# Kernel optimization log

Hardware: AMD Instinct MI355X
Metric: run time of the kernel (lower is better)

## Reference

```python
import jax, jax.numpy as jnp
import numpy as np

BN_EPS = 1e-5

def _vq(x, embed):
    # x: (..., dim), embed: (dim, K). Nearest-codeword lookup with straight-through.
    dim = x.shape[-1]
    flat = x.reshape(-1, dim)
    dist = (flat * flat).sum(1, keepdims=True) - 2.0 * (flat @ embed) + (embed * embed).sum(0, keepdims=True)
    ids = jnp.argmin(dist, axis=1)
    q = jnp.take(embed.T, ids, axis=0).reshape(x.shape)
    diff = jnp.mean((jax.lax.stop_gradient(q) - x) ** 2)
    q = x + jax.lax.stop_gradient(q - x)
    return q, diff

def _weight_quantize(W, embed, in_mem, out_mem):
    # W: (out_f, in_f). Group W.T into (out_g, in_g, in_mem*out_mem) blocks,
    # VQ each block, scatter back to (out_f, in_f). Matches torch chunk/stack loops.
    out_f, in_f = W.shape
    in_g, out_g = in_f // in_mem, out_f // out_mem
    g = W.T.reshape(in_g, in_mem, out_g, out_mem).transpose(2, 0, 1, 3).reshape(out_g, in_g, in_mem * out_mem)
    q, diff = _vq(g, embed)
    qW = q.reshape(out_g, in_g, in_mem, out_mem).transpose(0, 3, 1, 2).reshape(out_f, in_f)
    return qW, diff

def _bn(x, gamma, beta):
    # training-mode BatchNorm1d: biased batch variance
    mu = x.mean(axis=0)
    var = ((x - mu) ** 2).mean(axis=0)
    return (x - mu) * jax.lax.rsqrt(var + BN_EPS) * gamma + beta


def setup_inputs() -> dict:
    key = jax.random.key(0)
    ks = jax.random.split(key, 8)
    B, D_IN, H, D_OUT, K = 65536, 784, 512, 10, 512
    s = 0.05
    return {
        "x": jax.random.normal(ks[0], (B, D_IN), jnp.float32),
        "W1": jax.random.normal(ks[1], (H, D_IN), jnp.float32) * s,
        "b1": jnp.zeros((H,), jnp.float32),
        "gamma1": jnp.ones((H,), jnp.float32),
        "beta1": jnp.zeros((H,), jnp.float32),
        "E1": jax.random.normal(ks[2], (28, K), jnp.float32) * s,  # dim = in_mem(7)*out_mem(4)
        "W2": jax.random.normal(ks[3], (H, H), jnp.float32) * s,
        "b2": jnp.zeros((H,), jnp.float32),
        "E2": jax.random.normal(ks[4], (16, K), jnp.float32) * s,  # dim = in_mem(16)*out_mem(1)
        "W3": jax.random.normal(ks[5], (D_OUT, H), jnp.float32) * s,
        "b3": jnp.zeros((D_OUT,), jnp.float32),
    }


def reference(x, W1, b1, gamma1, beta1, E1, W2, b2, E2, W3, b3):
    qW1, diff1 = _weight_quantize(W1, E1, 7, 4)
    h = jax.nn.relu(x @ qW1.T + b1)
    qW2, diff2 = _weight_quantize(W2, E2, 16, 1)
    h = jax.nn.relu(_bn(h, gamma1, beta1) @ qW2.T + b2)
    out = h @ W3.T + b3
    return out, diff1 + diff2
```

## Files before the change

### kernel.cpp

```cpp
#include <hip/hip_runtime.h>
#include <stdint.h>

#define BATCH   65536
#define D_IN    784
#define KP      832
#define HDIM    512
#define D_OUT   10
#define NCODE   512
#define HT_LD   520

typedef _Float16 f16;
typedef _Float16 f16x8 __attribute__((ext_vector_type(8)));
typedef float    f32x4 __attribute__((ext_vector_type(4)));

__device__ __forceinline__ void gld_lds16(const void* g, void* l) {
  __builtin_amdgcn_global_load_lds((const __attribute__((address_space(1))) void*)g,
                                   (__attribute__((address_space(3))) void*)l, 16, 0, 0);
}

#define MEMFENCE asm volatile("" ::: "memory")
#define BARRIER() do { MEMFENCE; __builtin_amdgcn_s_barrier(); MEMFENCE; } while (0)

__global__ void k_vq1(const float* __restrict__ W1, const float* __restrict__ E1,
                      f16* __restrict__ qW1, float* __restrict__ diffacc) {
  #pragma clang fp contract(off)
  __shared__ float E1s[28 * NCODE];
  __shared__ float Ts[NCODE];
  for (int i = threadIdx.x; i < 28 * NCODE; i += 256) E1s[i] = E1[i];
  __syncthreads();
  for (int k = threadIdx.x; k < NCODE; k += 256) {
    float e0 = E1s[k];
    float t = e0 * e0;
    for (int j = 1; j < 28; ++j) {
      float e = E1s[j * NCODE + k];
      float ee = e * e;
      t = t + ee;
    }
    Ts[k] = t;
  }
  __syncthreads();
  const int wid = threadIdx.x >> 6, lane = threadIdx.x & 63;
  const int bid = blockIdx.x * 4 + wid;
  const int og = bid / 112, ig = bid % 112;
  float v[28], vv[28];
  #pragma unroll
  for (int j = 0; j < 28; ++j) {
    int om = j & 3, im = j >> 2;
    v[j] = W1[(og * 4 + om) * D_IN + ig * 7 + im];
    vv[j] = v[j] * v[j];
  }
  float r[8];
  #pragma unroll
  for (int j = 0; j < 8; ++j) r[j] = vv[j];
  #pragma unroll
  for (int j = 0; j < 8; ++j) r[j] = r[j] + vv[8 + j];
  #pragma unroll
  for (int j = 0; j < 8; ++j) r[j] = r[j] + vv[16 + j];
  float s = ((r[0] + r[1]) + (r[2] + r[3])) + ((r[4] + r[5]) + (r[6] + r[7]));
  s = s + vv[24]; s = s + vv[25]; s = s + vv[26]; s = s + vv[27];

  float bestd = 1e30f; int bestk = 0x7fffffff;
  for (int t = 0; t < 8; ++t) {
    int k = t * 64 + lane;
    float dot = 0.f;
    #pragma unroll
    for (int j = 0; j < 28; ++j) dot = __builtin_fmaf(v[j], E1s[j * NCODE + k], dot);
    float d = (s - 2.0f * dot) + Ts[k];
    if (d < bestd || (d == bestd && k < bestk)) { bestd = d; bestk = k; }
  }
  for (int off = 32; off; off >>= 1) {
    float d2 = __shfl_down(bestd, off, 64);
    int   k2 = __shfl_down(bestk, off, 64);
    if (d2 < bestd || (d2 == bestd && k2 < bestk)) { bestd = d2; bestk = k2; }
  }
  int kstar = __shfl(bestk, 0, 64);
  float sq = 0.f;
  if (lane < 28) {
    int om = lane & 3, im = lane >> 2;
    float q = E1s[lane * NCODE + kstar];
    qW1[(size_t)(og * 4 + om) * KP + ig * 7 + im] = (f16)q;
    float dd = q - v[lane]; sq = dd * dd;
  }
  for (int off = 32; off; off >>= 1) sq += __shfl_down(sq, off, 64);
  if (lane == 0) atomicAdd(&diffacc[bid & 127], sq);
}

__global__ void k_vq2(const float* __restrict__ W2, const float* __restrict__ E2,
                      f16* __restrict__ qW2, float* __restrict__ diffacc) {
  #pragma clang fp contract(off)
  __shared__ float E2s[16 * NCODE];
  __shared__ float Ts[NCODE];
  for (int i = threadIdx.x; i < 16 * NCODE; i += 256) E2s[i] = E2[i];
  __syncthreads();
  for (int k = threadIdx.x; k < NCODE; k += 256) {
    float e0 = E2s[k];
    float t = e0 * e0;
    for (int j = 1; j < 16; ++j) {
      float e = E2s[j * NCODE + k];
      float ee = e * e;
      t = t + ee;
    }
    Ts[k] = t;
  }
  __syncthreads();
  const int wid = threadIdx.x >> 6, lane = threadIdx.x & 63;
  const int bid = blockIdx.x * 4 + wid;
  const int og = bid >> 5, ig = bid & 31;
  float v[16], vv[16];
  #pragma unroll
  for (int j = 0; j < 16; ++j) {
    v[j] = W2[og * HDIM + ig * 16 + j];
    vv[j] = v[j] * v[j];
  }
  float r[8];
  #pragma unroll
  for (int j = 0; j < 8; ++j) r[j] = vv[j];
  #pragma unroll
  for (int j = 0; j < 8; ++j) r[j] = r[j] + vv[8 + j];
  float s = ((r[0] + r[1]) + (r[2] + r[3])) + ((r[4] + r[5]) + (r[6] + r[7]));

  float bestd = 1e30f; int bestk = 0x7fffffff;
  for (int t = 0; t < 8; ++t) {
    int k = t * 64 + lane;
    float dot = 0.f;
    #pragma unroll
    for (int j = 0; j < 16; ++j) dot = __builtin_fmaf(v[j], E2s[j * NCODE + k], dot);
    float d = (s - 2.0f * dot) + Ts[k];
    if (d < bestd || (d == bestd && k < bestk)) { bestd = d; bestk = k; }
  }
  for (int off = 32; off; off >>= 1) {
    float d2 = __shfl_down(bestd, off, 64);
    int   k2 = __shfl_down(bestk, off, 64);
    if (d2 < bestd || (d2 == bestd && k2 < bestk)) { bestd = d2; bestk = k2; }
  }
  int kstar = __shfl(bestk, 0, 64);
  float sq = 0.f;
  if (lane < 16) {
    float q = E2s[lane * NCODE + kstar];
    qW2[(size_t)og * HDIM + ig * 16 + lane] = (f16)q;
    float dd = q - v[lane]; sq = dd * dd;
  }
  for (int off = 32; off; off >>= 1) sq += __shfl_down(sq, off, 64);
  if (lane == 0) atomicAdd(&diffacc[bid & 127], sq);
}

__global__ void __launch_bounds__(512, 2)
k_gemm1(const float* __restrict__ X, const f16* __restrict__ Bw,
        const float* __restrict__ bias, f16* __restrict__ C,
        float* __restrict__ statacc) {
  __shared__ __align__(16) char lds_all[147456];
  __shared__ float cls[512], cls2[512];
  f16* ht = (f16*)lds_all;
  const int tid = threadIdx.x;
  const int bm = blockIdx.x;
  const int lane = tid & 63, wid = tid >> 6;
  const int waveM = wid & 1, waveN = wid >> 1;
  const int l15 = lane & 15, quad = lane >> 4;

  cls[tid] = 0.f; cls2[tid] = 0.f;

  const int rA = tid >> 2, cA = tid & 3;
  const float* gArow = X + (size_t)(bm * 128 + rA) * D_IN;
  const int wA0 = rA * 64 + ((cA ^ (rA & 7)) * 8);
  const int wA1 = rA * 64 + (((cA + 4) ^ (rA & 7)) * 8);
  const f16* gBp[8]; int lBoff[8];
  #pragma unroll
  for (int i = 0; i < 8; ++i) {
    int s = tid + i * 512;
    int rB = s >> 3, cB = s & 7;
    gBp[i] = Bw + (size_t)rB * KP + ((cB ^ (rB & 7)) * 8);
    lBoff[i] = s * 8;
  }

  f32x4 acc[4][8];
  #pragma unroll
  for (int i = 0; i < 4; ++i)
    #pragma unroll
    for (int j = 0; j < 8; ++j) acc[i][j] = (f32x4){0.f, 0.f, 0.f, 0.f};

  const int swz = (l15 & 7);
  const int arow = waveM * 64 + l15;
  const int brow = waveN * 128 + l15;

  float4 ra0, ra1, ra2, ra3;
  auto issueA = [&](int k0) {
    int g0 = k0 + cA * 8;
    int g1 = k0 + (cA + 4) * 8;
    int g0c = g0 < D_IN ? g0 : 0;
    int g1c = g1 < D_IN ? g1 : 0;
    ra0 = *(const float4*)(gArow + g0c);
    ra1 = *(const float4*)(gArow + g0c + 4);
    ra2 = *(const float4*)(gArow + g1c);
    ra3 = *(const float4*)(gArow + g1c + 4);
  };
  auto writeA = [&](int k0) {
    float4 a0 = ra0, a1 = ra1, b0 = ra2, b1 = ra3;
    if (k0 + cA * 8 >= D_IN)       { a0 = (float4){0.f,0.f,0.f,0.f}; a1 = a0; }
    if (k0 + (cA + 4) * 8 >= D_IN) { b0 = (float4){0.f,0.f,0.f,0.f}; b1 = b0; }
    f16x8 o0, o1;
    o0[0]=(f16)a0.x; o0[1]=(f16)a0.y; o0[2]=(f16)a0.z; o0[3]=(f16)a0.w;
    o0[4]=(f16)a1.x; o0[5]=(f16)a1.y; o0[6]=(f16)a1.z; o0[7]=(f16)a1.w;
    o1[0]=(f16)b0.x; o1[1]=(f16)b0.y; o1[2]=(f16)b0.z; o1[3]=(f16)b0.w;
    o1[4]=(f16)b1.x; o1[5]=(f16)b1.y; o1[6]=(f16)b1.z; o1[7]=(f16)b1.w;
    *(f16x8*)((f16*)lds_all + wA0) = o0;
    *(f16x8*)((f16*)lds_all + wA1) = o1;
  };
  auto issueB = [&](int k0, int bOff) {
    f16* Bs_ = (f16*)(lds_all + bOff);
    #pragma unroll
    for (int i = 0; i < 8; ++i) gld_lds16(gBp[i] + k0, Bs_ + lBoff[i]);
  };
  auto mma = [&](int bOff) {
    const f16* As_ = (const f16*)lds_all;
    const f16* Bs_ = (const f16*)(lds_all + bOff);
    #pragma unroll
    for (int ks = 0; ks < 2; ++ks) {
      const int coff = ((ks * 4 + quad) ^ swz) * 8;
      f16x8 af[4], bf[8];
      #pragma unroll
      for (int i = 0; i < 4; ++i) af[i] = *(const f16x8*)(As_ + (arow + i * 16) * 64 + coff);
      #pragma unroll
      for (int j = 0; j < 8; ++j) bf[j] = *(const f16x8*)(Bs_ + (brow + j * 16) * 64 + coff);
      #pragma unroll
      for (int i = 0; i < 4; ++i)
        #pragma unroll
        for (int j = 0; j < 8; ++j)
          acc[i][j] = __builtin_amdgcn_mfma_f32_16x16x32_f16(af[i], bf[j], acc[i][j], 0, 0, 0);
    }
  };

  const int NT = KP / 64;
  issueA(0);  MEMFENCE;
  issueB(0, 16384); MEMFENCE;

  for (int k = 0; k < NT; ++k) {
    BARRIER();
    writeA(k * 64);
    MEMFENCE;
    if (k + 1 < NT) {
      issueA((k + 1) * 64); MEMFENCE;
      issueB((k + 1) * 64, 16384 + ((k + 1) & 1) * 65536); MEMFENCE;
      asm volatile("s_waitcnt vmcnt(12) lgkmcnt(0)" ::: "memory");
    } else {
      asm volatile("s_waitcnt vmcnt(0) lgkmcnt(0)" ::: "memory");
    }
    BARRIER();
    __builtin_amdgcn_s_setprio(1);
    mma(16384 + (k & 1) * 65536);
    __builtin_amdgcn_s_setprio(0);
  }
  __syncthreads();

  const int colbase = waveN * 128 + l15;
  float bcol[8];
  #pragma unroll
  for (int j = 0; j < 8; ++j) bcol[j] = bias[colbase + j * 16];
  float cs[8], cs2[8];
  #pragma unroll
  for (int j = 0; j < 8; ++j) { cs[j] = 0.f; cs2[j] = 0.f; }
  #pragma unroll
  for (int i = 0; i < 4; ++i)
    #pragma unroll
    for (int r2 = 0; r2 < 4; ++r2) {
      int rloc = waveM * 64 + i * 16 + quad * 4 + r2;
      #pragma unroll
      for (int j = 0; j < 8; ++j) {
        float v = acc[i][j][r2] + bcol[j];
        v = v > 0.f ? v : 0.f;
        ht[rloc * HT_LD + waveN * 128 + j * 16 + l15] = (f16)v;
        cs[j] += v; cs2[j] += v * v;
      }
    }
  #pragma unroll
  for (int j = 0; j < 8; ++j) {
    cs[j]  += __shfl_xor(cs[j], 16, 64);  cs[j]  += __shfl_xor(cs[j], 32, 64);
    cs2[j] += __shfl_xor(cs2[j], 16, 64); cs2[j] += __shfl_xor(cs2[j], 32, 64);
  }
  if (quad == 0) {
    #pragma unroll
    for (int j = 0; j < 8; ++j) {
      atomicAdd(&cls[waveN * 128 + j * 16 + l15], cs[j]);
      atomicAdd(&cls2[waveN * 128 + j * 16 + l15], cs2[j]);
    }
  }
  __syncthreads();
  atomicAdd(&statacc[256 + tid], cls[tid]);
  atomicAdd(&statacc[768 + tid], cls2[tid]);
  #pragma unroll
  for (int rr = 0; rr < 16; ++rr) {
    int row = wid * 16 + rr;
    f16x8 vrow = *(const f16x8*)(ht + row * HT_LD + lane * 8);
    *(f16x8*)(C + (size_t)(bm * 128 + row) * HDIM + lane * 8) = vrow;
  }
}

__global__ void k_bnprep(const float* __restrict__ acc, const float* __restrict__ gamma,
                         const float* __restrict__ beta, float* __restrict__ ab,
                         const float* __restrict__ W3, f16* __restrict__ W3h,
                         float* __restrict__ diff_out) {
  const int c = threadIdx.x;
  const float inv = 1.f / 65536.f;
  float mu = acc[256 + c] * inv;
  float msq = acc[768 + c] * inv;
  float var = msq - mu * mu;
  float a = gamma[c] / sqrtf(var + 1e-5f);
  ab[c] = a;
  ab[512 + c] = beta[c] - mu * a;
  #pragma unroll
  for (int o = 0; o < 16; ++o)
    W3h[o * HDIM + c] = (o < D_OUT) ? (f16)W3[o * HDIM + c] : (f16)0.f;
  if (c == 0) {
    float s1 = 0.f, s2 = 0.f;
    for (int i = 0; i < 128; ++i) { s1 += acc[i]; s2 += acc[128 + i]; }
    diff_out[0] = s1 * (1.f / 401408.f) + s2 * (1.f / 262144.f);
  }
}

__global__ void k_bnfold(f16* __restrict__ qW2, const float* __restrict__ ab,
                         const float* __restrict__ b2, float* __restrict__ bias2) {
  __shared__ float red[256];
  const int n = blockIdx.x, t = threadIdx.x;
  float partial = 0.f;
  #pragma unroll
  for (int kk = 0; kk < 2; ++kk) {
    int k = t + kk * 256;
    float w = (float)qW2[n * HDIM + k];
    partial += ab[512 + k] * w;
    qW2[n * HDIM + k] = (f16)(ab[k] * w);
  }
  red[t] = partial; __syncthreads();
  for (int s = 128; s > 0; s >>= 1) { if (t < s) red[t] += red[t + s]; __syncthreads(); }
  if (t == 0) bias2[n] = b2[n] + red[0];
}

__global__ void __launch_bounds__(512, 2)
k_gemm2f(const f16* __restrict__ A, const f16* __restrict__ Bw,
         const float* __restrict__ bias2, const f16* __restrict__ W3h,
         const float* __restrict__ b3, float* __restrict__ out) {
  __shared__ __align__(16) char lds_all[147456];
  f16* ht = (f16*)lds_all;
  const int tid = threadIdx.x;
  const int bm = blockIdx.x;
  const int lane = tid & 63, wid = tid >> 6;
  const int waveM = wid & 1, waveN = wid >> 1;
  const int l15 = lane & 15, quad = lane >> 4;

  const int rA = tid >> 2, cA = tid & 3;
  const f16* gArow = A + (size_t)(bm * 128 + rA) * HDIM;
  const int wA0 = rA * 64 + ((cA ^ (rA & 7)) * 8);
  const int wA1 = rA * 64 + (((cA + 4) ^ (rA & 7)) * 8);
  const f16* gBp[8]; int lBoff[8];
  #pragma unroll
  for (int i = 0; i < 8; ++i) {
    int s = tid + i * 512;
    int rB = s >> 3, cB = s & 7;
    gBp[i] = Bw + (size_t)rB * HDIM + ((cB ^ (rB & 7)) * 8);
    lBoff[i] = s * 8;
  }

  f32x4 acc[4][8];
  #pragma unroll
  for (int i = 0; i < 4; ++i)
    #pragma unroll
    for (int j = 0; j < 8; ++j) acc[i][j] = (f32x4){0.f, 0.f, 0.f, 0.f};

  const int swz = (l15 & 7);
  const int arow = waveM * 64 + l15;
  const int brow = waveN * 128 + l15;

  f16x8 ra0, ra1;
  auto issueA = [&](int k0) {
    ra0 = *(const f16x8*)(gArow + k0 + cA * 8);
    ra1 = *(const f16x8*)(gArow + k0 + (cA + 4) * 8);
  };
  auto writeA = [&]() {
    *(f16x8*)((f16*)lds_all + wA0) = ra0;
    *(f16x8*)((f16*)lds_all + wA1) = ra1;
  };
  auto issueB = [&](int k0, int bOff) {
    f16* Bs_ = (f16*)(lds_all + bOff);
    #pragma unroll
    for (int i = 0; i < 8; ++i) gld_lds16(gBp[i] + k0, Bs_ + lBoff[i]);
  };
  auto mma = [&](int bOff) {
    const f16* As_ = (const f16*)lds_all;
    const f16* Bs_ = (const f16*)(lds_all + bOff);
    #pragma unroll
    for (int ks = 0; ks < 2; ++ks) {
      const int coff = ((ks * 4 + quad) ^ swz) * 8;
      f16x8 af[4], bf[8];
      #pragma unroll
      for (int i = 0; i < 4; ++i) af[i] = *(const f16x8*)(As_ + (arow + i * 16) * 64 + coff);
      #pragma unroll
      for (int j = 0; j < 8; ++j) bf[j] = *(const f16x8*)(Bs_ + (brow + j * 16) * 64 + coff);
      #pragma unroll
      for (int i = 0; i < 4; ++i)
        #pragma unroll
        for (int j = 0; j < 8; ++j)
          acc[i][j] = __builtin_amdgcn_mfma_f32_16x16x32_f16(af[i], bf[j], acc[i][j], 0, 0, 0);
    }
  };

  const int NT = HDIM / 64;
  issueA(0);  MEMFENCE;
  issueB(0, 16384); MEMFENCE;

  for (int k = 0; k < NT; ++k) {
    BARRIER();
    writeA();
    MEMFENCE;
    if (k + 1 < NT) {
      issueA((k + 1) * 64); MEMFENCE;
      issueB((k + 1) * 64, 16384 + ((k + 1) & 1) * 65536); MEMFENCE;
      asm volatile("s_waitcnt vmcnt(10) lgkmcnt(0)" ::: "memory");
    } else {
      asm volatile("s_waitcnt vmcnt(0) lgkmcnt(0)" ::: "memory");
    }
    BARRIER();
    __builtin_amdgcn_s_setprio(1);
    mma(16384 + (k & 1) * 65536);
    __builtin_amdgcn_s_setprio(0);
  }
  __syncthreads();

  const int colbase = waveN * 128 + l15;
  float bcol[8];
  #pragma unroll
  for (int j = 0; j < 8; ++j) bcol[j] = bias2[colbase + j * 16];
  #pragma unroll
  for (int i = 0; i < 4; ++i)
    #pragma unroll
    for (int r2 = 0; r2 < 4; ++r2) {
      int rloc = waveM * 64 + i * 16 + quad * 4 + r2;
      #pragma unroll
      for (int j = 0; j < 8; ++j) {
        float v = acc[i][j][r2] + bcol[j];
        v = v > 0.f ? v : 0.f;
        ht[rloc * HT_LD + waveN * 128 + j * 16 + l15] = (f16)v;
      }
    }
  __syncthreads();
  f32x4 oacc = (f32x4){0.f, 0.f, 0.f, 0.f};
  #pragma unroll
  for (int ks = 0; ks < 16; ++ks) {
    f16x8 bfr = *(const f16x8*)(W3h + l15 * HDIM + ks * 32 + quad * 8);
    f16x8 afr = *(const f16x8*)(ht + (wid * 16 + l15) * HT_LD + ks * 32 + quad * 8);
    oacc = __builtin_amdgcn_mfma_f32_16x16x32_f16(afr, bfr, oacc, 0, 0, 0);
  }
  if (l15 < D_OUT) {
    float badd = b3[l15];
    #pragma unroll
    for (int r2 = 0; r2 < 4; ++r2) {
      int row = bm * 128 + wid * 16 + quad * 4 + r2;
      out[(size_t)row * D_OUT + l15] = oacc[r2] + badd;
    }
  }
}

extern "C" void kernel_launch(void* const* d_in, const int* in_sizes, int n_in,
                              void* d_out, int out_size, void* d_ws, size_t ws_size,
                              hipStream_t stream) {
  const float* x     = (const float*)d_in[0];
  const float* W1    = (const float*)d_in[1];
  const float* b1    = (const float*)d_in[2];
  const float* gamma = (const float*)d_in[3];
  const float* beta  = (const float*)d_in[4];
  const float* E1    = (const float*)d_in[5];
  const float* W2    = (const float*)d_in[6];
  const float* b2    = (const float*)d_in[7];
  const float* E2    = (const float*)d_in[8];
  const float* W3    = (const float*)d_in[9];
  const float* b3    = (const float*)d_in[10];
  float* out = (float*)d_out;

  char* ws = (char*)d_ws;
  float* accum = (float*)ws;
  f16* qW1h = (f16*)(ws + 8192);
  f16* qW2h = (f16*)(ws + 860160);
  f16* W3h  = (f16*)(ws + 1384448);
  float* ab = (float*)(ws + 1400832);
  float* bias2 = (float*)(ws + 1404928);
  f16* h    = (f16*)(ws + 1409024);

  (void)hipMemsetAsync(ws, 0, 860160, stream);
  k_vq1<<<3584, 256, 0, stream>>>(W1, E1, qW1h, accum);
  k_vq2<<<4096, 256, 0, stream>>>(W2, E2, qW2h, accum + 128);
  k_gemm1<<<512, 512, 0, stream>>>(x, qW1h, b1, h, accum);
  k_bnprep<<<1, 512, 0, stream>>>(accum, gamma, beta, ab, W3, W3h, out + (size_t)BATCH * D_OUT);
  k_bnfold<<<512, 256, 0, stream>>>(qW2h, ab, b2, bias2);
  k_gemm2f<<<512, 512, 0, stream>>>(h, qW2h, bias2, W3h, b3, out);
}
```

Measured before the change: 515.1 us.

## Merge VQ kernels, fold BN prep into bnfold, finer-grained GEMM pipelining

```diff
diff --git a/kernel.cpp b/kernel.cpp
--- a/kernel.cpp
+++ b/kernel.cpp
@@ -20,128 +20,126 @@
 
 #define MEMFENCE asm volatile("" ::: "memory")
 #define BARRIER() do { MEMFENCE; __builtin_amdgcn_s_barrier(); MEMFENCE; } while (0)
-
-__global__ void k_vq1(const float* __restrict__ W1, const float* __restrict__ E1,
-                      f16* __restrict__ qW1, float* __restrict__ diffacc) {
+#define LGKM0 asm volatile("s_waitcnt lgkmcnt(0)" ::: "memory")
+
+__global__ void k_vq(const float* __restrict__ W1, const float* __restrict__ E1,
+                     f16* __restrict__ qW1,
+                     const float* __restrict__ W2, const float* __restrict__ E2,
+                     f16* __restrict__ qW2, float* __restrict__ diffacc) {
   #pragma clang fp contract(off)
-  __shared__ float E1s[28 * NCODE];
+  __shared__ float Es[28 * NCODE];
   __shared__ float Ts[NCODE];
-  for (int i = threadIdx.x; i < 28 * NCODE; i += 256) E1s[i] = E1[i];
-  __syncthreads();
-  for (int k = threadIdx.x; k < NCODE; k += 256) {
-    float e0 = E1s[k];
-    float t = e0 * e0;
-    for (int j = 1; j < 28; ++j) {
-      float e = E1s[j * NCODE + k];
-      float ee = e * e;
-      t = t + ee;
-    }
-    Ts[k] = t;
-  }
-  __syncthreads();
   const int wid = threadIdx.x >> 6, lane = threadIdx.x & 63;
-  const int bid = blockIdx.x * 4 + wid;
-  const int og = bid / 112, ig = bid % 112;
-  float v[28], vv[28];
-  #pragma unroll
-  for (int j = 0; j < 28; ++j) {
-    int om = j & 3, im = j >> 2;
-    v[j] = W1[(og * 4 + om) * D_IN + ig * 7 + im];
-    vv[j] = v[j] * v[j];
-  }
-  float r[8];
-  #pragma unroll
-  for (int j = 0; j < 8; ++j) r[j] = vv[j];
-  #pragma unroll
-  for (int j = 0; j < 8; ++j) r[j] = r[j] + vv[8 + j];
-  #pragma unroll
-  for (int j = 0; j < 8; ++j) r[j] = r[j] + vv[16 + j];
-  float s = ((r[0] + r[1]) + (r[2] + r[3])) + ((r[4] + r[5]) + (r[6] + r[7]));
-  s = s + vv[24]; s = s + vv[25]; s = s + vv[26]; s = s + vv[27];
-
-  float bestd = 1e30f; int bestk = 0x7fffffff;
-  for (int t = 0; t < 8; ++t) {
-    int k = t * 64 + lane;
-    float dot = 0.f;
-    #pragma unroll
-    for (int j = 0; j < 28; ++j) dot = __builtin_fmaf(v[j], E1s[j * NCODE + k], dot);
-    float d = (s - 2.0f * dot) + Ts[k];
-    if (d < bestd || (d == bestd && k < bestk)) { bestd = d; bestk = k; }
-  }
-  for (int off = 32; off; off >>= 1) {
-    float d2 = __shfl_down(bestd, off, 64);
-    int   k2 = __shfl_down(bestk, off, 64);
-    if (d2 < bestd || (d2 == bestd && k2 < bestk)) { bestd = d2; bestk = k2; }
-  }
-  int kstar = __shfl(bestk, 0, 64);
-  float sq = 0.f;
-  if (lane < 28) {
-    int om = lane & 3, im = lane >> 2;
-    float q = E1s[lane * NCODE + kstar];
-    qW1[(size_t)(og * 4 + om) * KP + ig * 7 + im] = (f16)q;
-    float dd = q - v[lane]; sq = dd * dd;
-  }
-  for (int off = 32; off; off >>= 1) sq += __shfl_down(sq, off, 64);
-  if (lane == 0) atomicAdd(&diffacc[bid & 127], sq);
-}
-
-__global__ void k_vq2(const float* __restrict__ W2, const float* __restrict__ E2,
-                      f16* __restrict__ qW2, float* __restrict__ diffacc) {
-  #pragma clang fp contract(off)
-  __shared__ float E2s[16 * NCODE];
-  __shared__ float Ts[NCODE];
-  for (int i = threadIdx.x; i < 16 * NCODE; i += 256) E2s[i] = E2[i];
-  __syncthreads();
-  for (int k = threadIdx.x; k < NCODE; k += 256) {
-    float e0 = E2s[k];
-    float t = e0 * e0;
-    for (int j = 1; j < 16; ++j) {
-      float e = E2s[j * NCODE + k];
-      float ee = e * e;
-      t = t + ee;
-    }
-    Ts[k] = t;
-  }
-  __syncthreads();
-  const int wid = threadIdx.x >> 6, lane = threadIdx.x & 63;
-  const int bid = blockIdx.x * 4 + wid;
-  const int og = bid >> 5, ig = bid & 31;
-  float v[16], vv[16];
-  #pragma unroll
-  for (int j = 0; j < 16; ++j) {
-    v[j] = W2[og * HDIM + ig * 16 + j];
-    vv[j] = v[j] * v[j];
-  }
-  float r[8];
-  #pragma unroll
-  for (int j = 0; j < 8; ++j) r[j] = vv[j];
-  #pragma unroll
-  for (int j = 0; j < 8; ++j) r[j] = r[j] + vv[8 + j];
-  float s = ((r[0] + r[1]) + (r[2] + r[3])) + ((r[4] + r[5]) + (r[6] + r[7]));
-
-  float bestd = 1e30f; int bestk = 0x7fffffff;
-  for (int t = 0; t < 8; ++t) {
-    int k = t * 64 + lane;
-    float dot = 0.f;
-    #pragma unroll
-    for (int j = 0; j < 16; ++j) dot = __builtin_fmaf(v[j], E2s[j * NCODE + k], dot);
-    float d = (s - 2.0f * dot) + Ts[k];
-    if (d < bestd || (d == bestd && k < bestk)) { bestd = d; bestk = k; }
-  }
-  for (int off = 32; off; off >>= 1) {
-    float d2 = __shfl_down(bestd, off, 64);
-    int   k2 = __shfl_down(bestk, off, 64);
-    if (d2 < bestd || (d2 == bestd && k2 < bestk)) { bestd = d2; bestk = k2; }
-  }
-  int kstar = __shfl(bestk, 0, 64);
-  float sq = 0.f;
-  if (lane < 16) {
-    float q = E2s[lane * NCODE + kstar];
-    qW2[(size_t)og * HDIM + ig * 16 + lane] = (f16)q;
-    float dd = q - v[lane]; sq = dd * dd;
-  }
-  for (int off = 32; off; off >>= 1) sq += __shfl_down(sq, off, 64);
-  if (lane == 0) atomicAdd(&diffacc[bid & 127], sq);
+  if (blockIdx.x < 3584) {
+    for (int i = threadIdx.x; i < 28 * NCODE; i += 256) Es[i] = E1[i];
+    __syncthreads();
+    for (int k = threadIdx.x; k < NCODE; k += 256) {
+      float e0 = Es[k];
+      float t = e0 * e0;
+      for (int j = 1; j < 28; ++j) {
+        float e = Es[j * NCODE + k];
+        float ee = e * e;
+        t = t + ee;
+      }
+      Ts[k] = t;
+    }
+    __syncthreads();
+    const int bid = blockIdx.x * 4 + wid;
+    const int og = bid / 112, ig = bid % 112;
+    float v[28], vv[28];
+    #pragma unroll
+    for (int j = 0; j < 28; ++j) {
+      int om = j & 3, im = j >> 2;
+      v[j] = W1[(og * 4 + om) * D_IN + ig * 7 + im];
+      vv[j] = v[j] * v[j];
+    }
+    float r[8];
+    #pragma unroll
+    for (int j = 0; j < 8; ++j) r[j] = vv[j];
+    #pragma unroll
+    for (int j = 0; j < 8; ++j) r[j] = r[j] + vv[8 + j];
+    #pragma unroll
+    for (int j = 0; j < 8; ++j) r[j] = r[j] + vv[16 + j];
+    float s = ((r[0] + r[1]) + (r[2] + r[3])) + ((r[4] + r[5]) + (r[6] + r[7]));
+    s = s + vv[24]; s = s + vv[25]; s = s + vv[26]; s = s + vv[27];
+
+    float bestd = 1e30f; int bestk = 0x7fffffff;
+    for (int t = 0; t < 8; ++t) {
+      int k = t * 64 + lane;
+      float dot = 0.f;
+      #pragma unroll
+      for (int j = 0; j < 28; ++j) dot = __builtin_fmaf(v[j], Es[j * NCODE + k], dot);
+      float d = (s - 2.0f * dot) + Ts[k];
+      if (d < bestd || (d == bestd && k < bestk)) { bestd = d; bestk = k; }
+    }
+    for (int off = 32; off; off >>= 1) {
+      float d2 = __shfl_down(bestd, off, 64);
+      int   k2 = __shfl_down(bestk, off, 64);
+      if (d2 < bestd || (d2 == bestd && k2 < bestk)) { bestd = d2; bestk = k2; }
+    }
+    int kstar = __shfl(bestk, 0, 64);
+    float sq = 0.f;
+    if (lane < 28) {
+      int om = lane & 3, im = lane >> 2;
+      float q = Es[lane * NCODE + kstar];
+      qW1[(size_t)(og * 4 + om) * KP + ig * 7 + im] = (f16)q;
+      float dd = q - v[lane]; sq = dd * dd;
+    }
+    for (int off = 32; off; off >>= 1) sq += __shfl_down(sq, off, 64);
+    if (lane == 0) atomicAdd(&diffacc[bid & 127], sq);
+  } else {
+    for (int i = threadIdx.x; i < 16 * NCODE; i += 256) Es[i] = E2[i];
+    __syncthreads();
+    for (int k = threadIdx.x; k < NCODE; k += 256) {
+      float e0 = Es[k];
+      float t = e0 * e0;
+      for (int j = 1; j < 16; ++j) {
+        float e = Es[j * NCODE + k];
+        float ee = e * e;
+        t = t + ee;
+      }
+      Ts[k] = t;
+    }
+    __syncthreads();
+    const int bid = (blockIdx.x - 3584) * 4 + wid;
+    const int og = bid >> 5, ig = bid & 31;
+    float v[16], vv[16];
+    #pragma unroll
+    for (int j = 0; j < 16; ++j) {
+      v[j] = W2[og * HDIM + ig * 16 + j];
+      vv[j] = v[j] * v[j];
+    }
+    float r[8];
+    #pragma unroll
+    for (int j = 0; j < 8; ++j) r[j] = vv[j];
+    #pragma unroll
+    for (int j = 0; j < 8; ++j) r[j] = r[j] + vv[8 + j];
+    float s = ((r[0] + r[1]) + (r[2] + r[3])) + ((r[4] + r[5]) + (r[6] + r[7]));
+
+    float bestd = 1e30f; int bestk = 0x7fffffff;
+    for (int t = 0; t < 8; ++t) {
+      int k = t * 64 + lane;
+      float dot = 0.f;
+      #pragma unroll
+      for (int j = 0; j < 16; ++j) dot = __builtin_fmaf(v[j], Es[j * NCODE + k], dot);
+      float d = (s - 2.0f * dot) + Ts[k];
+      if (d < bestd || (d == bestd && k < bestk)) { bestd = d; bestk = k; }
+    }
+    for (int off = 32; off; off >>= 1) {
+      float d2 = __shfl_down(bestd, off, 64);
+      int   k2 = __shfl_down(bestk, off, 64);
+      if (d2 < bestd || (d2 == bestd && k2 < bestk)) { bestd = d2; bestk = k2; }
+    }
+    int kstar = __shfl(bestk, 0, 64);
+    float sq = 0.f;
+    if (lane < 16) {
+      float q = Es[lane * NCODE + kstar];
+      qW2[(size_t)og * HDIM + ig * 16 + lane] = (f16)q;
+      float dd = q - v[lane]; sq = dd * dd;
+    }
+    for (int off = 32; off; off >>= 1) sq += __shfl_down(sq, off, 64);
+    if (lane == 0) atomicAdd(&diffacc[128 + (bid & 127)], sq);
+  }
 }
 
 __global__ void __launch_bounds__(512, 2)
@@ -149,15 +147,14 @@
         const float* __restrict__ bias, f16* __restrict__ C,
         float* __restrict__ statacc) {
   __shared__ __align__(16) char lds_all[147456];
-  __shared__ float cls[512], cls2[512];
   f16* ht = (f16*)lds_all;
+  float* cls  = (float*)(lds_all + 137216);
+  float* cls2 = (float*)(lds_all + 139264);
   const int tid = threadIdx.x;
   const int bm = blockIdx.x;
   const int lane = tid & 63, wid = tid >> 6;
   const int waveM = wid & 1, waveN = wid >> 1;
   const int l15 = lane & 15, quad = lane >> 4;
-
-  cls[tid] = 0.f; cls2[tid] = 0.f;
 
   const int rA = tid >> 2, cA = tid & 3;
   const float* gArow = X + (size_t)(bm * 128 + rA) * D_IN;
@@ -205,52 +202,69 @@
     *(f16x8*)((f16*)lds_all + wA0) = o0;
     *(f16x8*)((f16*)lds_all + wA1) = o1;
   };
-  auto issueB = [&](int k0, int bOff) {
+  auto issueB4 = [&](int k0, int bOff, int half) {
     f16* Bs_ = (f16*)(lds_all + bOff);
     #pragma unroll
-    for (int i = 0; i < 8; ++i) gld_lds16(gBp[i] + k0, Bs_ + lBoff[i]);
-  };
-  auto mma = [&](int bOff) {
+    for (int i = 0; i < 4; ++i) gld_lds16(gBp[half * 4 + i] + k0, Bs_ + lBoff[half * 4 + i]);
+  };
+  auto rdA = [&](int ks, f16x8 (&af)[4]) {
     const f16* As_ = (const f16*)lds_all;
+    const int coff = ((ks * 4 + quad) ^ swz) * 8;
+    #pragma unroll
+    for (int i = 0; i < 4; ++i) af[i] = *(const f16x8*)(As_ + (arow + i * 16) * 64 + coff);
+  };
+  auto rdB = [&](int bOff, int ks, int j0, f16x8 (&bf)[4]) {
     const f16* Bs_ = (const f16*)(lds_all + bOff);
-    #pragma unroll
-    for (int ks = 0; ks < 2; ++ks) {
-      const int coff = ((ks * 4 + quad) ^ swz) * 8;
-      f16x8 af[4], bf[8];
-      #pragma unroll
-      for (int i = 0; i < 4; ++i) af[i] = *(const f16x8*)(As_ + (arow + i * 16) * 64 + coff);
-      #pragma unroll
-      for (int j = 0; j < 8; ++j) bf[j] = *(const f16x8*)(Bs_ + (brow + j * 16) * 64 + coff);
-      #pragma unroll
-      for (int i = 0; i < 4; ++i)
-        #pragma unroll
-        for (int j = 0; j < 8; ++j)
-          acc[i][j] = __builtin_amdgcn_mfma_f32_16x16x32_f16(af[i], bf[j], acc[i][j], 0, 0, 0);
-    }
+    const int coff = ((ks * 4 + quad) ^ swz) * 8;
+    #pragma unroll
+    for (int j = 0; j < 4; ++j) bf[j] = *(const f16x8*)(Bs_ + (brow + (j0 + j) * 16) * 64 + coff);
+  };
+  auto mm16 = [&](const f16x8 (&af)[4], const f16x8 (&bf)[4], int j0) {
+    #pragma unroll
+    for (int i = 0; i < 4; ++i)
+      #pragma unroll
+      for (int j = 0; j < 4; ++j)
+        acc[i][j0 + j] = __builtin_amdgcn_mfma_f32_16x16x32_f16(af[i], bf[j], acc[i][j0 + j], 0, 0, 0);
   };
 
   const int NT = KP / 64;
-  issueA(0);  MEMFENCE;
-  issueB(0, 16384); MEMFENCE;
+  issueA(0); MEMFENCE;
+  issueB4(0, 16384, 0); issueB4(0, 16384, 1); MEMFENCE;
+  writeA(0); MEMFENCE;
+  asm volatile("s_waitcnt vmcnt(0) lgkmcnt(0)" ::: "memory");
+  BARRIER();
 
   for (int k = 0; k < NT; ++k) {
-    BARRIER();
-    writeA(k * 64);
+    const int bOff = 16384 + (k & 1) * 65536;
+    const int nOff = 16384 + ((k + 1) & 1) * 65536;
+    const bool more = (k + 1 < NT);
+    f16x8 af0[4], af1[4], bf[4];
+    rdA(0, af0); rdA(1, af1); rdB(bOff, 0, 0, bf);
+    if (more) { issueA((k + 1) * 64); MEMFENCE; issueB4((k + 1) * 64, nOff, 0); }
+    BARRIER(); LGKM0;
+    __builtin_amdgcn_s_setprio(1); mm16(af0, bf, 0); __builtin_amdgcn_s_setprio(0);
+    BARRIER();
+    rdB(bOff, 0, 4, bf);
+    if (more) issueB4((k + 1) * 64, nOff, 1);
+    BARRIER(); LGKM0;
+    __builtin_amdgcn_s_setprio(1); mm16(af0, bf, 4); __builtin_amdgcn_s_setprio(0);
+    BARRIER();
+    rdB(bOff, 1, 0, bf);
+    if (more) writeA((k + 1) * 64);
+    BARRIER(); LGKM0;
+    __builtin_amdgcn_s_setprio(1); mm16(af1, bf, 0); __builtin_amdgcn_s_setprio(0);
+    BARRIER();
+    rdB(bOff, 1, 4, bf);
     MEMFENCE;
-    if (k + 1 < NT) {
-      issueA((k + 1) * 64); MEMFENCE;
-      issueB((k + 1) * 64, 16384 + ((k + 1) & 1) * 65536); MEMFENCE;
-      asm volatile("s_waitcnt vmcnt(12) lgkmcnt(0)" ::: "memory");
-    } else {
-      asm volatile("s_waitcnt vmcnt(0) lgkmcnt(0)" ::: "memory");
-    }
-    BARRIER();
-    __builtin_amdgcn_s_setprio(1);
-    mma(16384 + (k & 1) * 65536);
-    __builtin_amdgcn_s_setprio(0);
+    if (more) asm volatile("s_waitcnt vmcnt(0)" ::: "memory");
+    BARRIER(); LGKM0;
+    __builtin_amdgcn_s_setprio(1); mm16(af1, bf, 4); __builtin_amdgcn_s_setprio(0);
+    BARRIER();
   }
   __syncthreads();
 
+  cls[tid] = 0.f; cls2[tid] = 0.f;
+  __syncthreads();
   const int colbase = waveN * 128 + l15;
   float bcol[8];
   #pragma unroll
@@ -294,43 +308,46 @@
   }
 }
 
-__global__ void k_bnprep(const float* __restrict__ acc, const float* __restrict__ gamma,
-                         const float* __restrict__ beta, float* __restrict__ ab,
+__global__ void k_bnfold(const float* __restrict__ acc, const float* __restrict__ gamma,
+                         const float* __restrict__ beta, const float* __restrict__ b2,
+                         f16* __restrict__ qW2, float* __restrict__ bias2,
                          const float* __restrict__ W3, f16* __restrict__ W3h,
                          float* __restrict__ diff_out) {
-  const int c = threadIdx.x;
+  __shared__ float ab_a[512], ab_b[512], red[256];
+  const int t = threadIdx.x, n = blockIdx.x;
   const float inv = 1.f / 65536.f;
-  float mu = acc[256 + c] * inv;
-  float msq = acc[768 + c] * inv;
-  float var = msq - mu * mu;
-  float a = gamma[c] / sqrtf(var + 1e-5f);
-  ab[c] = a;
-  ab[512 + c] = beta[c] - mu * a;
-  #pragma unroll
-  for (int o = 0; o < 16; ++o)
-    W3h[o * HDIM + c] = (o < D_OUT) ? (f16)W3[o * HDIM + c] : (f16)0.f;
-  if (c == 0) {
-    float s1 = 0.f, s2 = 0.f;
-    for (int i = 0; i < 128; ++i) { s1 += acc[i]; s2 += acc[128 + i]; }
-    diff_out[0] = s1 * (1.f / 401408.f) + s2 * (1.f / 262144.f);
-  }
-}
-
-__global__ void k_bnfold(f16* __restrict__ qW2, const float* __restrict__ ab,
-                         const float* __restrict__ b2, float* __restrict__ bias2) {
-  __shared__ float red[256];
-  const int n = blockIdx.x, t = threadIdx.x;
+  for (int c = t; c < 512; c += 256) {
+    float mu = acc[256 + c] * inv;
+    float msq = acc[768 + c] * inv;
+    float var = msq - mu * mu;
+    float a = gamma[c] / sqrtf(var + 1e-5f);
+    ab_a[c] = a;
+    ab_b[c] = beta[c] - mu * a;
+  }
+  __syncthreads();
   float partial = 0.f;
   #pragma unroll
   for (int kk = 0; kk < 2; ++kk) {
     int k = t + kk * 256;
     float w = (float)qW2[n * HDIM + k];
-    partial += ab[512 + k] * w;
-    qW2[n * HDIM + k] = (f16)(ab[k] * w);
+    partial += ab_b[k] * w;
+    qW2[n * HDIM + k] = (f16)(ab_a[k] * w);
   }
   red[t] = partial; __syncthreads();
   for (int s = 128; s > 0; s >>= 1) { if (t < s) red[t] += red[t + s]; __syncthreads(); }
   if (t == 0) bias2[n] = b2[n] + red[0];
+  if (n == 0) {
+    for (int c = t; c < 512; c += 256) {
+      #pragma unroll
+      for (int o = 0; o < 16; ++o)
+        W3h[o * HDIM + c] = (o < D_OUT) ? (f16)W3[o * HDIM + c] : (f16)0.f;
+    }
+    if (t == 0) {
+      float s1 = 0.f, s2 = 0.f;
+      for (int i = 0; i < 128; ++i) { s1 += acc[i]; s2 += acc[128 + i]; }
+      diff_out[0] = s1 * (1.f / 401408.f) + s2 * (1.f / 262144.f);
+    }
+  }
 }
 
 __global__ void __launch_bounds__(512, 2)
@@ -377,49 +394,64 @@
     *(f16x8*)((f16*)lds_all + wA0) = ra0;
     *(f16x8*)((f16*)lds_all + wA1) = ra1;
   };
-  auto issueB = [&](int k0, int bOff) {
+  auto issueB4 = [&](int k0, int bOff, int half) {
     f16* Bs_ = (f16*)(lds_all + bOff);
     #pragma unroll
-    for (int i = 0; i < 8; ++i) gld_lds16(gBp[i] + k0, Bs_ + lBoff[i]);
-  };
-  auto mma = [&](int bOff) {
+    for (int i = 0; i < 4; ++i) gld_lds16(gBp[half * 4 + i] + k0, Bs_ + lBoff[half * 4 + i]);
+  };
+  auto rdA = [&](int ks, f16x8 (&af)[4]) {
     const f16* As_ = (const f16*)lds_all;
+    const int coff = ((ks * 4 + quad) ^ swz) * 8;
+    #pragma unroll
+    for (int i = 0; i < 4; ++i) af[i] = *(const f16x8*)(As_ + (arow + i * 16) * 64 + coff);
+  };
+  auto rdB = [&](int bOff, int ks, int j0, f16x8 (&bf)[4]) {
     const f16* Bs_ = (const f16*)(lds_all + bOff);
-    #pragma unroll
-    for (int ks = 0; ks < 2; ++ks) {
-      const int coff = ((ks * 4 + quad) ^ swz) * 8;
-      f16x8 af[4], bf[8];
-      #pragma unroll
-      for (int i = 0; i < 4; ++i) af[i] = *(const f16x8*)(As_ + (arow + i * 16) * 64 + coff);
-      #pragma unroll
-      for (int j = 0; j < 8; ++j) bf[j] = *(const f16x8*)(Bs_ + (brow + j * 16) * 64 + coff);
-      #pragma unroll
-      for (int i = 0; i < 4; ++i)
-        #pragma unroll
-        for (int j = 0; j < 8; ++j)
-          acc[i][j] = __builtin_amdgcn_mfma_f32_16x16x32_f16(af[i], bf[j], acc[i][j], 0, 0, 0);
-    }
+    const int coff = ((ks * 4 + quad) ^ swz) * 8;
+    #pragma unroll
+    for (int j = 0; j < 4; ++j) bf[j] = *(const f16x8*)(Bs_ + (brow + (j0 + j) * 16) * 64 + coff);
+  };
+  auto mm16 = [&](const f16x8 (&af)[4], const f16x8 (&bf)[4], int j0) {
+    #pragma unroll
+    for (int i = 0; i < 4; ++i)
+      #pragma unroll
+      for (int j = 0; j < 4; ++j)
+        acc[i][j0 + j] = __builtin_amdgcn_mfma_f32_16x16x32_f16(af[i], bf[j], acc[i][j0 + j], 0, 0, 0);
   };
 
   const int NT = HDIM / 64;
-  issueA(0);  MEMFENCE;
-  issueB(0, 16384); MEMFENCE;
+  issueA(0); MEMFENCE;
+  issueB4(0, 16384, 0); issueB4(0, 16384, 1); MEMFENCE;
+  writeA(); MEMFENCE;
+  asm volatile("s_waitcnt vmcnt(0) lgkmcnt(0)" ::: "memory");
+  BARRIER();
 
   for (int k = 0; k < NT; ++k) {
-    BARRIER();
-    writeA();
+    const int bOff = 16384 + (k & 1) * 65536;
+    const int nOff = 16384 + ((k + 1) & 1) * 65536;
+    const bool more = (k + 1 < NT);
+    f16x8 af0[4], af1[4], bf[4];
+    rdA(0, af0); rdA(1, af1); rdB(bOff, 0, 0, bf);
+    if (more) { issueA((k + 1) * 64); MEMFENCE; issueB4((k + 1) * 64, nOff, 0); }
+    BARRIER(); LGKM0;
+    __builtin_amdgcn_s_setprio(1); mm16(af0, bf, 0); __builtin_amdgcn_s_setprio(0);
+    BARRIER();
+    rdB(bOff, 0, 4, bf);
+    if (more) issueB4((k + 1) * 64, nOff, 1);
+    BARRIER(); LGKM0;
+    __builtin_amdgcn_s_setprio(1); mm16(af0, bf, 4); __builtin_amdgcn_s_setprio(0);
+    BARRIER();
+    rdB(bOff, 1, 0, bf);
+    if (more) writeA();
+    BARRIER(); LGKM0;
+    __builtin_amdgcn_s_setprio(1); mm16(af1, bf, 0); __builtin_amdgcn_s_setprio(0);
+    BARRIER();
+    rdB(bOff, 1, 4, bf);
     MEMFENCE;
-    if (k + 1 < NT) {
-      issueA((k + 1) * 64); MEMFENCE;
-      issueB((k + 1) * 64, 16384 + ((k + 1) & 1) * 65536); MEMFENCE;
-      asm volatile("s_waitcnt vmcnt(10) lgkmcnt(0)" ::: "memory");
-    } else {
-      asm volatile("s_waitcnt vmcnt(0) lgkmcnt(0)" ::: "memory");
-    }
-    BARRIER();
-    __builtin_amdgcn_s_setprio(1);
-    mma(16384 + (k & 1) * 65536);
-    __builtin_amdgcn_s_setprio(0);
+    if (more) asm volatile("s_waitcnt vmcnt(0)" ::: "memory");
+    BARRIER(); LGKM0;
+    __builtin_amdgcn_s_setprio(1); mm16(af1, bf, 4); __builtin_amdgcn_s_setprio(0);
+    BARRIER();
   }
   __syncthreads();
 
@@ -478,15 +510,13 @@
   f16* qW1h = (f16*)(ws + 8192);
   f16* qW2h = (f16*)(ws + 860160);
   f16* W3h  = (f16*)(ws + 1384448);
-  float* ab = (float*)(ws + 1400832);
   float* bias2 = (float*)(ws + 1404928);
   f16* h    = (f16*)(ws + 1409024);
 
   (void)hipMemsetAsync(ws, 0, 860160, stream);
-  k_vq1<<<3584, 256, 0, stream>>>(W1, E1, qW1h, accum);
-  k_vq2<<<4096, 256, 0, stream>>>(W2, E2, qW2h, accum + 128);
+  k_vq<<<7680, 256, 0, stream>>>(W1, E1, qW1h, W2, E2, qW2h, accum);
   k_gemm1<<<512, 512, 0, stream>>>(x, qW1h, b1, h, accum);
-  k_bnprep<<<1, 512, 0, stream>>>(accum, gamma, beta, ab, W3, W3h, out + (size_t)BATCH * D_OUT);
-  k_bnfold<<<512, 256, 0, stream>>>(qW2h, ab, b2, bias2);
+  k_bnfold<<<512, 256, 0, stream>>>(accum, gamma, beta, b2, qW2h, bias2, W3, W3h,
+                                    out + (size_t)BATCH * D_OUT);
   k_gemm2f<<<512, 512, 0, stream>>>(h, qW2h, bias2, W3h, b3, out);
 }
```

Result: no change. 521.7 us (+1.3%).
